# Kernel tuning notes

Measured on AMD Instinct MI355X. Metric: run time of the kernel, lower is better.

The kernel has to match this reference:

```python
import jax, jax.numpy as jnp
import numpy as np

SLOPE = 0.2
NEG = -9e15

def setup_inputs() -> dict:
    key = jax.random.key(0)
    k1, k2, k3, k4 = jax.random.split(key, 4)
    N, INP, OUT = 8192, 512, 128
    h = jax.random.normal(k1, (N, INP), dtype=jnp.float32)
    adj = jax.random.randint(k2, (N, N), 0, 2, dtype=jnp.int32)
    W = jax.random.normal(k3, (INP, OUT), dtype=jnp.float32) * (1.0 / np.sqrt(INP))
    a = jax.random.normal(k4, (2 * OUT,), dtype=jnp.float32) * (1.0 / np.sqrt(2 * OUT))
    return {"h": h, "adj": adj, "W": W, "a": a}

def reference(h, adj, W, a):
    OUT = W.shape[1]
    Wh = h @ W                               # [N, out]
    # a . [Wh_i, Wh_j] decomposes into two matvecs (same math as pairwise concat)
    f1 = Wh @ a[:OUT]                        # [N]
    f2 = Wh @ a[OUT:]                        # [N]
    e = jax.nn.leaky_relu(f1[:, None] + f2[None, :], negative_slope=SLOPE)  # [N, N]
    scores = jnp.where(adj > 0, e, NEG)
    attention = jax.nn.softmax(scores, axis=1)
    return attention @ Wh                    # [N, out]
```

## Files before the change

### kernel.cpp

```cpp
#include <hip/hip_runtime.h>

typedef unsigned short u16;
typedef unsigned int u32;
typedef __attribute__((ext_vector_type(8))) short short8v;
typedef __attribute__((ext_vector_type(4))) short short4v;
typedef __attribute__((ext_vector_type(4))) float float4v;
typedef __attribute__((ext_vector_type(4))) int   int4v;

#define N_NODES 8192
#define D_IN    512
#define D_OUT   128
#define SLOPEF  0.2f
#define LOG2E   1.4426950408889634f
#define NSEG    4
#define SEGCOLS 2048
#define NCHUNK  16
#define ROWS    64

static __device__ __forceinline__ u16 f2bf(float f) {
    union { float f; unsigned int i; } v; v.f = f;
    unsigned int r = v.i + 0x7fff + ((v.i >> 16) & 1);
    return (u16)(r >> 16);
}
static __device__ __forceinline__ void lds_barrier() {
    asm volatile("s_waitcnt lgkmcnt(0)" ::: "memory");
    __builtin_amdgcn_s_barrier();
    asm volatile("" ::: "memory");
}

__global__ __launch_bounds__(256) void kc_convert(
        const float* __restrict__ h, const float* __restrict__ W,
        u16* __restrict__ hb, u16* __restrict__ WbT)
{
    if (blockIdx.x < 2048) {
        const size_t t = (size_t)blockIdx.x * 256 + threadIdx.x;
        const float4v* src = (const float4v*)h + t * 2;
        const float4v v0 = src[0], v1 = src[1];
        short8v o;
        o[0] = (short)f2bf(v0[0]); o[1] = (short)f2bf(v0[1]);
        o[2] = (short)f2bf(v0[2]); o[3] = (short)f2bf(v0[3]);
        o[4] = (short)f2bf(v1[0]); o[5] = (short)f2bf(v1[1]);
        o[6] = (short)f2bf(v1[2]); o[7] = (short)f2bf(v1[3]);
        *(short8v*)(hb + t * 8) = o;
    } else {
        const int t2 = (blockIdx.x - 2048) * 256 + threadIdx.x;
        const int k = t2 >> 4;
        const int n0 = (t2 & 15) * 8;
        const float4v* src = (const float4v*)(W + (size_t)k * D_OUT + n0);
        const float4v v0 = src[0], v1 = src[1];
        #pragma unroll
        for (int e = 0; e < 4; e++) WbT[(size_t)(n0 + e) * D_IN + k] = f2bf(v0[e]);
        #pragma unroll
        for (int e = 0; e < 4; e++) WbT[(size_t)(n0 + 4 + e) * D_IN + k] = f2bf(v1[e]);
    }
}

__global__ __launch_bounds__(256) void k1m_proj(
        const u16* __restrict__ hb, const u16* __restrict__ WbT,
        const float* __restrict__ a, u16* __restrict__ WhT,
        float* __restrict__ f1, float* __restrict__ f2)
{
    __shared__ short As[32 * 136];
    __shared__ short Ws[128 * 136];
    __shared__ float pf1[32][65];
    __shared__ float pf2[32][65];

    const int tid = threadIdx.x;
    const int rowbase = blockIdx.x * 32;
    const int lane = tid & 63, w = tid >> 6;
    const int quad = lane >> 4, m16 = lane & 15;

    float4v acc[2][2];
    #pragma unroll
    for (int mt = 0; mt < 2; mt++)
        #pragma unroll
        for (int nt = 0; nt < 2; nt++) {
            acc[mt][nt][0] = 0.f; acc[mt][nt][1] = 0.f;
            acc[mt][nt][2] = 0.f; acc[mt][nt][3] = 0.f;
        }

    for (int c = 0; c < 4; c++) {
        const int kc0 = c * 128;
        if (c) __syncthreads();
        {
            const int row = tid >> 3, koff = (tid & 7) * 16;
            const short8v* src = (const short8v*)(hb + (size_t)(rowbase + row) * D_IN + kc0 + koff);
            const short8v s0 = src[0], s1 = src[1];
            *(short8v*)&As[row * 136 + koff] = s0;
            *(short8v*)&As[row * 136 + koff + 8] = s1;
        }
        {
            const int n = tid & 127, h2 = tid >> 7;
            #pragma unroll
            for (int i = 0; i < 8; i++) {
                const int koff = h2 * 64 + i * 8;
                *(short8v*)&Ws[n * 136 + koff] =
                    *(const short8v*)(WbT + (size_t)n * D_IN + kc0 + koff);
            }
        }
        __syncthreads();
        #pragma unroll
        for (int ks = 0; ks < 4; ks++) {
            const int ko = ks * 32 + quad * 8;
            const short8v af0 = *(const short8v*)&As[m16 * 136 + ko];
            const short8v af1 = *(const short8v*)&As[(16 + m16) * 136 + ko];
            const short8v bf0 = *(const short8v*)&Ws[(w * 32 + m16) * 136 + ko];
            const short8v bf1 = *(const short8v*)&Ws[(w * 32 + 16 + m16) * 136 + ko];
            acc[0][0] = __builtin_amdgcn_mfma_f32_16x16x32_bf16(af0, bf0, acc[0][0], 0, 0, 0);
            acc[0][1] = __builtin_amdgcn_mfma_f32_16x16x32_bf16(af0, bf1, acc[0][1], 0, 0, 0);
            acc[1][0] = __builtin_amdgcn_mfma_f32_16x16x32_bf16(af1, bf0, acc[1][0], 0, 0, 0);
            acc[1][1] = __builtin_amdgcn_mfma_f32_16x16x32_bf16(af1, bf1, acc[1][1], 0, 0, 0);
        }
    }

    #pragma unroll
    for (int mt = 0; mt < 2; mt++) {
        #pragma unroll
        for (int nt = 0; nt < 2; nt++) {
            const int n = w * 32 + nt * 16 + m16;
            short4v p;
            #pragma unroll
            for (int reg = 0; reg < 4; reg++) p[reg] = (short)f2bf(acc[mt][nt][reg]);
            *(short4v*)(WhT + (size_t)n * N_NODES + rowbase + mt * 16 + quad * 4) = p;
        }
    }

    float a1v[2], a2v[2];
    #pragma unroll
    for (int nt = 0; nt < 2; nt++) {
        a1v[nt] = a[w * 32 + nt * 16 + m16];
        a2v[nt] = a[D_OUT + w * 32 + nt * 16 + m16];
    }
    #pragma unroll
    for (int mt = 0; mt < 2; mt++)
        #pragma unroll
        for (int reg = 0; reg < 4; reg++) {
            const int row = mt * 16 + quad * 4 + reg;
            pf1[row][w * 16 + m16] = acc[mt][0][reg] * a1v[0] + acc[mt][1][reg] * a1v[1];
            pf2[row][w * 16 + m16] = acc[mt][0][reg] * a2v[0] + acc[mt][1][reg] * a2v[1];
        }
    __syncthreads();
    if (tid < 32) {
        float s = 0.f;
        #pragma unroll
        for (int j = 0; j < 64; j++) s += pf1[tid][j];
        f1[rowbase + tid] = s * LOG2E;
    } else if (tid < 64) {
        float s = 0.f;
        #pragma unroll
        for (int j = 0; j < 64; j++) s += pf2[tid - 32][j];
        f2[rowbase + tid - 32] = s * LOG2E;
    }
}

__global__ __launch_bounds__(256, 2) void k2_attn(
        const int* __restrict__ adj, const u16* __restrict__ WhT,
        const float* __restrict__ f1g, const float* __restrict__ f2g,
        float* __restrict__ numw, float* __restrict__ denw)
{
    __shared__ short Pt[2][ROWS * 136];
    __shared__ float f2s[2304];
    __shared__ float f1s[ROWS];
    __shared__ float rs[ROWS][5];
    __shared__ float ssum[ROWS];

    const int tid = threadIdx.x;
    const int rb  = blockIdx.x >> 2;
    const int seg = blockIdx.x & 3;
    const int rowbase = rb * ROWS;
    const int colbase = seg * SEGCOLS;
    const int r = tid >> 2, g = tid & 3;
    const int lane = tid & 63, w = tid >> 6;
    const int quad = lane >> 4, m16 = lane & 15;

    if (tid < ROWS) f1s[tid] = f1g[rowbase + tid];
    #pragma unroll
    for (int i = 0; i < 2; i++) {
        const int idx = (tid + 256 * i) * 4;
        *(float4v*)&f2s[idx + ((idx >> 5) << 2)] = *(const float4v*)&f2g[colbase + idx];
    }

    const int4v* arow = (const int4v*)(adj + (size_t)(rowbase + r) * N_NODES + colbase);
    int4v a4[8];
    #pragma unroll
    for (int i = 0; i < 8; i++) a4[i] = arow[g * 8 + i];

    float4v acc[4][2];
    #pragma unroll
    for (int mt = 0; mt < 4; mt++)
        #pragma unroll
        for (int nt = 0; nt < 2; nt++) {
            acc[mt][nt][0] = 0.f; acc[mt][nt][1] = 0.f;
            acc[mt][nt][2] = 0.f; acc[mt][nt][3] = 0.f;
        }
    float ls0 = 0.f, ls1 = 0.f, ls2 = 0.f, ls3 = 0.f;

    __syncthreads();

    const float f1v = f1s[r];

    auto weight_phase = [&](int jc, short* ptb) {
        const float* f2p = &f2s[jc * 144 + g * 36];
        u32 packed[16];
        #pragma unroll
        for (int i = 0; i < 8; i++) {
            const float4v fv = *(const float4v*)&f2p[i * 4];
            const int4v av = a4[i];
            u32 wb[4];
            #pragma unroll
            for (int e = 0; e < 4; e++) {
                const u32 msk = (av[e] > 0) ? 0xffff0000u : 0u;
                float x = f1v + fv[e];
                x = fmaxf(x, SLOPEF * x);
                const float ex = __builtin_amdgcn_exp2f(x);
                const u32 wt = __float_as_uint(ex) & msk;
                wb[e] = wt;
                if (e == 0) ls0 += __uint_as_float(wt);
                else if (e == 1) ls1 += __uint_as_float(wt);
                else if (e == 2) ls2 += __uint_as_float(wt);
                else ls3 += __uint_as_float(wt);
            }
            packed[i * 2]     = __builtin_amdgcn_perm(wb[1], wb[0], 0x07060302);
            packed[i * 2 + 1] = __builtin_amdgcn_perm(wb[3], wb[2], 0x07060302);
        }
        int* pdst = (int*)(ptb + r * 136 + g * 32);
        #pragma unroll
        for (int q = 0; q < 4; q++) {
            int4v st;
            st[0] = (int)packed[q * 4 + 0]; st[1] = (int)packed[q * 4 + 1];
            st[2] = (int)packed[q * 4 + 2]; st[3] = (int)packed[q * 4 + 3];
            *(int4v*)&pdst[q * 4] = st;
        }
    };

    weight_phase(0, Pt[0]);
    #pragma unroll
    for (int i = 0; i < 8; i++) a4[i] = arow[32 + g * 8 + i];

    #pragma unroll 2
    for (int jc = 0; jc < NCHUNK; jc++) {
        lds_barrier();

        {
            const u16* b0p = WhT + (size_t)(w * 32 + m16) * N_NODES + colbase + jc * 128 + quad * 8;
            const u16* b1p = b0p + 16 * N_NODES;
            const short* ap = &Pt[jc & 1][m16 * 136 + quad * 8];
            #pragma unroll
            for (int ks = 0; ks < 4; ks++) {
                const int ko = ks * 32;
                const short8v bv0 = *(const short8v*)(b0p + ko);
                const short8v bv1 = *(const short8v*)(b1p + ko);
                #pragma unroll
                for (int mt = 0; mt < 4; mt++) {
                    const short8v af = *(const short8v*)(ap + mt * 16 * 136 + ko);
                    acc[mt][0] = __builtin_amdgcn_mfma_f32_16x16x32_bf16(af, bv0, acc[mt][0], 0, 0, 0);
                    acc[mt][1] = __builtin_amdgcn_mfma_f32_16x16x32_bf16(af, bv1, acc[mt][1], 0, 0, 0);
                }
            }
        }
        if (jc + 1 < NCHUNK) {
            weight_phase(jc + 1, Pt[(jc + 1) & 1]);
            if (jc + 2 < NCHUNK) {
                #pragma unroll
                for (int i = 0; i < 8; i++) a4[i] = arow[(jc + 2) * 32 + g * 8 + i];
            }
        }
    }

    rs[r][g] = (ls0 + ls1) + (ls2 + ls3);
    __syncthreads();
    if (tid < ROWS) {
        float s = 0.f;
        #pragma unroll
        for (int j = 0; j < 4; j++) s += rs[tid][j];
        ssum[tid] = s;
        denw[(size_t)(rowbase + tid) * NSEG + seg] = s;
    }
    __syncthreads();

    #pragma unroll
    for (int mt = 0; mt < 4; mt++) {
        #pragma unroll
        for (int nt = 0; nt < 2; nt++) {
            const int cl = w * 32 + nt * 16 + m16;
            #pragma unroll
            for (int reg = 0; reg < 4; reg++) {
                const int rl = mt * 16 + quad * 4 + reg;
                numw[((size_t)(rowbase + rl) * NSEG + seg) * D_OUT + cl] = acc[mt][nt][reg];
            }
        }
    }
}

__global__ __launch_bounds__(256) void k3_reduce(
        const float* __restrict__ numw, const float* __restrict__ denw,
        float* __restrict__ out)
{
    const int tid = threadIdx.x;
    const int row = blockIdx.x * 2 + (tid >> 7);
    const int c   = tid & 127;
    float s = 0.f, d = 0.f;
    #pragma unroll
    for (int sg = 0; sg < NSEG; sg++) {
        s += numw[((size_t)row * NSEG + sg) * D_OUT + c];
        d += denw[(size_t)row * NSEG + sg];
    }
    out[(size_t)row * D_OUT + c] = s / d;
}

extern "C" void kernel_launch(void* const* d_in, const int* in_sizes, int n_in,
                              void* d_out, int out_size, void* d_ws, size_t ws_size,
                              hipStream_t stream) {
    const float* h   = (const float*)d_in[0];
    const int*   adj = (const int*)d_in[1];
    const float* W   = (const float*)d_in[2];
    const float* a   = (const float*)d_in[3];

    char* ws = (char*)d_ws;
    u16*   hb   = (u16*)ws;
    u16*   WbT  = (u16*)(ws + (size_t)8 * 1024 * 1024);
    u16*   WhT  = (u16*)(ws + (size_t)9 * 1024 * 1024);
    float* f1   = (float*)(ws + (size_t)11 * 1024 * 1024);
    float* f2   = f1 + N_NODES;
    float* numw = (float*)(ws + (size_t)12 * 1024 * 1024);
    float* denw = (float*)(ws + (size_t)28 * 1024 * 1024);

    kc_convert<<<2080, 256, 0, stream>>>(h, W, hb, WbT);
    k1m_proj<<<N_NODES / 32, 256, 0, stream>>>(hb, WbT, a, WhT, f1, f2);
    k2_attn<<<(N_NODES / ROWS) * NSEG, 256, 0, stream>>>(adj, WhT, f1, f2, numw, denw);
    k3_reduce<<<N_NODES / 2, 256, 0, stream>>>(numw, denw, (float*)d_out);
}
```

Baseline: 397.7 us.

## Retile attention kernel to 128-row, 512-thread blocks over eight column segments

The attention kernel now processes 128 rows per block with 512 threads, splits columns into eight 1024-wide segments instead of four 2048-wide ones, and gives each wave a 16-column output slice across eight M tiles. This reuses each loaded WhT B fragment across more rows, which cuts global traffic for WhT per output, and raises parallelism in the grid. The cost is twice as much partial numerator and denominator data written and reduced in the final pass, a larger LDS tile that may limit occupancy, and more accumulator registers per thread.

```diff
diff --git a/kernel.cpp b/kernel.cpp
--- a/kernel.cpp
+++ b/kernel.cpp
@@ -12,10 +12,10 @@
 #define D_OUT   128
 #define SLOPEF  0.2f
 #define LOG2E   1.4426950408889634f
-#define NSEG    4
-#define SEGCOLS 2048
-#define NCHUNK  16
-#define ROWS    64
+#define NSEG    8
+#define SEGCOLS 1024
+#define NCHUNK  8
+#define ROWS    128
 
 static __device__ __forceinline__ u16 f2bf(float f) {
     union { float f; unsigned int i; } v; v.f = f;
@@ -153,20 +153,19 @@
     }
 }
 
-__global__ __launch_bounds__(256, 2) void k2_attn(
+__global__ __launch_bounds__(512, 4) void k2_attn(
         const int* __restrict__ adj, const u16* __restrict__ WhT,
         const float* __restrict__ f1g, const float* __restrict__ f2g,
         float* __restrict__ numw, float* __restrict__ denw)
 {
     __shared__ short Pt[2][ROWS * 136];
-    __shared__ float f2s[2304];
+    __shared__ float f2s[1152];
     __shared__ float f1s[ROWS];
     __shared__ float rs[ROWS][5];
-    __shared__ float ssum[ROWS];
 
     const int tid = threadIdx.x;
-    const int rb  = blockIdx.x >> 2;
-    const int seg = blockIdx.x & 3;
+    const int rb  = blockIdx.x >> 3;
+    const int seg = blockIdx.x & 7;
     const int rowbase = rb * ROWS;
     const int colbase = seg * SEGCOLS;
     const int r = tid >> 2, g = tid & 3;
@@ -174,9 +173,8 @@
     const int quad = lane >> 4, m16 = lane & 15;
 
     if (tid < ROWS) f1s[tid] = f1g[rowbase + tid];
-    #pragma unroll
-    for (int i = 0; i < 2; i++) {
-        const int idx = (tid + 256 * i) * 4;
+    if (tid < 256) {
+        const int idx = tid * 4;
         *(float4v*)&f2s[idx + ((idx >> 5) << 2)] = *(const float4v*)&f2g[colbase + idx];
     }
 
@@ -185,14 +183,11 @@
     #pragma unroll
     for (int i = 0; i < 8; i++) a4[i] = arow[g * 8 + i];
 
-    float4v acc[4][2];
-    #pragma unroll
-    for (int mt = 0; mt < 4; mt++)
-        #pragma unroll
-        for (int nt = 0; nt < 2; nt++) {
-            acc[mt][nt][0] = 0.f; acc[mt][nt][1] = 0.f;
-            acc[mt][nt][2] = 0.f; acc[mt][nt][3] = 0.f;
-        }
+    float4v acc[8];
+    #pragma unroll
+    for (int mt = 0; mt < 8; mt++) {
+        acc[mt][0] = 0.f; acc[mt][1] = 0.f; acc[mt][2] = 0.f; acc[mt][3] = 0.f;
+    }
     float ls0 = 0.f, ls1 = 0.f, ls2 = 0.f, ls3 = 0.f;
 
     __syncthreads();
@@ -242,19 +237,16 @@
         lds_barrier();
 
         {
-            const u16* b0p = WhT + (size_t)(w * 32 + m16) * N_NODES + colbase + jc * 128 + quad * 8;
-            const u16* b1p = b0p + 16 * N_NODES;
+            const u16* bp = WhT + (size_t)(w * 16 + m16) * N_NODES + colbase + jc * 128 + quad * 8;
             const short* ap = &Pt[jc & 1][m16 * 136 + quad * 8];
             #pragma unroll
             for (int ks = 0; ks < 4; ks++) {
                 const int ko = ks * 32;
-                const short8v bv0 = *(const short8v*)(b0p + ko);
-                const short8v bv1 = *(const short8v*)(b1p + ko);
+                const short8v bv = *(const short8v*)(bp + ko);
                 #pragma unroll
-                for (int mt = 0; mt < 4; mt++) {
+                for (int mt = 0; mt < 8; mt++) {
                     const short8v af = *(const short8v*)(ap + mt * 16 * 136 + ko);
-                    acc[mt][0] = __builtin_amdgcn_mfma_f32_16x16x32_bf16(af, bv0, acc[mt][0], 0, 0, 0);
-                    acc[mt][1] = __builtin_amdgcn_mfma_f32_16x16x32_bf16(af, bv1, acc[mt][1], 0, 0, 0);
+                    acc[mt] = __builtin_amdgcn_mfma_f32_16x16x32_bf16(af, bv, acc[mt], 0, 0, 0);
                 }
             }
         }
@@ -273,21 +265,16 @@
         float s = 0.f;
         #pragma unroll
         for (int j = 0; j < 4; j++) s += rs[tid][j];
-        ssum[tid] = s;
         denw[(size_t)(rowbase + tid) * NSEG + seg] = s;
     }
-    __syncthreads();
-
-    #pragma unroll
-    for (int mt = 0; mt < 4; mt++) {
-        #pragma unroll
-        for (int nt = 0; nt < 2; nt++) {
-            const int cl = w * 32 + nt * 16 + m16;
-            #pragma unroll
-            for (int reg = 0; reg < 4; reg++) {
-                const int rl = mt * 16 + quad * 4 + reg;
-                numw[((size_t)(rowbase + rl) * NSEG + seg) * D_OUT + cl] = acc[mt][nt][reg];
-            }
+
+    const int cl = w * 16 + m16;
+    #pragma unroll
+    for (int mt = 0; mt < 8; mt++) {
+        #pragma unroll
+        for (int reg = 0; reg < 4; reg++) {
+            const int rl = mt * 16 + quad * 4 + reg;
+            numw[((size_t)(rowbase + rl) * NSEG + seg) * D_OUT + cl] = acc[mt][reg];
         }
     }
 }
@@ -323,10 +310,10 @@
     float* f1   = (float*)(ws + (size_t)11 * 1024 * 1024);
     float* f2   = f1 + N_NODES;
     float* numw = (float*)(ws + (size_t)12 * 1024 * 1024);
-    float* denw = (float*)(ws + (size_t)28 * 1024 * 1024);
+    float* denw = (float*)(ws + (size_t)44 * 1024 * 1024);
 
     kc_convert<<<2080, 256, 0, stream>>>(h, W, hb, WbT);
     k1m_proj<<<N_NODES / 32, 256, 0, stream>>>(hb, WbT, a, WhT, f1, f2);
-    k2_attn<<<(N_NODES / ROWS) * NSEG, 256, 0, stream>>>(adj, WhT, f1, f2, numw, denw);
+    k2_attn<<<(N_NODES / ROWS) * NSEG, 512, 0, stream>>>(adj, WhT, f1, f2, numw, denw);
     k3_reduce<<<N_NODES / 2, 256, 0, stream>>>(numw, denw, (float*)d_out);
 }
```

After: 404.8 us. No clear change (+1.8%).
